# Kernel optimization log

Hardware: AMD Instinct MI355X
Metric: run time of the kernel (lower is better)

## Reference

```python
import jax, jax.numpy as jnp
import numpy as np

CLIP = 16          # relative_clip
REL = 2 * CLIP + 1 # relative_size = 33
NEG = 1e9


def setup_inputs() -> dict:
    key = jax.random.key(0)
    k1, k2, k3, k4, k5 = jax.random.split(key, 5)
    B, L, D = 8, 2048, 64
    return {
        "query": jax.random.normal(k1, (B, L, D), jnp.float32),
        "key": jax.random.normal(k2, (B, L, D), jnp.float32),
        "value": jax.random.normal(k3, (B, L, D), jnp.float32),
        "mask": jnp.ones((B, 1, L), jnp.float32),
        "key_relative": jax.random.normal(k4, (REL, D), jnp.float32),
        "value_relative": jax.random.normal(k5, (REL, D), jnp.float32),
    }


def reference(query, key, value, mask, key_relative, value_relative):
    B, Q, Dk = query.shape
    K = key.shape[1]
    scale = jnp.asarray(np.sqrt(Dk), query.dtype)

    # dot products [B,Q,K] (torch code does broadcast-mul+sum; matmul is same math)
    dot = jnp.einsum('bqd,bkd->bqk', query, key)

    # relative key bias: dot_relative [B,Q,REL], gathered by diag_id[q,k]
    dot_rel = jnp.einsum('bqd,td->bqt', query, key_relative)
    qi = jnp.arange(Q)[:, None]
    kj = jnp.arange(K)[None, :]
    diag_id = jnp.clip(qi - kj + CLIP, 0, 2 * CLIP)           # [Q,K]
    rel_bias = jnp.take_along_axis(
        dot_rel, jnp.broadcast_to(diag_id[None], (B, Q, K)), axis=2)
    dot = dot + rel_bias

    # only_attend_front: causal mask (strict upper triangle penalized)
    causal = jnp.triu(jnp.ones((K, K), dot.dtype), 1) * NEG   # [K,K]
    dot = dot - causal[None]

    # padding mask (broadcast)
    dot = dot - (1.0 - mask) * NEG

    logits = dot / scale
    probs = jax.nn.softmax(logits, axis=-1)
    # zero rows where every position is masked out
    n_masked = jnp.sum(dot <= -5e8, axis=-1, keepdims=True)
    probs = probs * (n_masked < K).astype(probs.dtype)
    # dropout with droprate=0.0 / eval mode -> identity

    res = jnp.einsum('bqk,bkd->bqd', probs, value)

    # relative value recombination: recover_id[q,r] = q + r - CLIP, OOB -> K (zero col)
    recover = jnp.arange(Q)[:, None] + jnp.arange(REL)[None, :] - CLIP  # [Q,REL]
    recover = jnp.where((recover < 0) | (recover >= K), K, recover)
    probs_pad = jnp.concatenate(
        [probs, jnp.zeros((B, Q, 1), probs.dtype)], axis=-1)           # [B,Q,K+1]
    rel_probs = jnp.take_along_axis(
        probs_pad, jnp.broadcast_to(recover[None], (B, Q, REL)), axis=2)
    res = res + jnp.einsum('bqr,rd->bqd', rel_probs, value_relative)
    return res
```

## Files before the change

### kernel.cpp

```cpp
#include <hip/hip_runtime.h>

typedef __attribute__((ext_vector_type(4))) float f32x4;
typedef __attribute__((ext_vector_type(8))) short s16x8;
typedef __attribute__((ext_vector_type(4))) short s16x4;

#define LSEQ 2048
#define NB   8
#define CH   8
#define UPB  80
#define NUNIT 640

#define QSCALE   0.180336880f
#define PENSCALE 1.8033688e8f

#define OFF_QB    0x000000u
#define OFF_KB    0x200000u
#define OFF_VTB   0x400000u
#define OFF_PEN   0x600000u
#define OFF_KREL  0x610000u
#define OFF_OPART 0x620000u
#define OFF_ML    0x1020000u

__device__ __forceinline__ unsigned short f2bf(float f) {
    union { float f; unsigned int u; } v; v.f = f;
    unsigned int u = v.u;
    return (unsigned short)((u + 0x7fffu + ((u >> 16) & 1u)) >> 16);
}

__device__ __forceinline__ float bf2f(unsigned short b) {
    union { unsigned int u; float f; } v; v.u = ((unsigned int)b) << 16;
    return v.f;
}

__global__ __launch_bounds__(256)
void convert_kernel(const float* __restrict__ Q, const float* __restrict__ K,
                    const float* __restrict__ V, const float* __restrict__ Msk,
                    const float* __restrict__ Krel, char* __restrict__ ws)
{
    const int tid = threadIdx.x;
    const int bid = blockIdx.x;
    unsigned short* Qb  = (unsigned short*)(ws + OFF_QB);
    unsigned short* Kb  = (unsigned short*)(ws + OFF_KB);
    unsigned short* VTb = (unsigned short*)(ws + OFF_VTB);
    float*          pen = (float*)(ws + OFF_PEN);
    unsigned short* Krb = (unsigned short*)(ws + OFF_KREL);

    if (bid < 1024) {
        int base = bid * 1024 + tid * 4;
        f32x4 q4 = *(const f32x4*)(Q + base);
        s16x4 o;
        o.x = (short)f2bf(q4.x * QSCALE); o.y = (short)f2bf(q4.y * QSCALE);
        o.z = (short)f2bf(q4.z * QSCALE); o.w = (short)f2bf(q4.w * QSCALE);
        *(s16x4*)(Qb + base) = o;
    } else if (bid < 2048) {
        int base = (bid - 1024) * 1024 + tid * 4;
        f32x4 k4 = *(const f32x4*)(K + base);
        s16x4 o;
        o.x = (short)f2bf(k4.x); o.y = (short)f2bf(k4.y);
        o.z = (short)f2bf(k4.z); o.w = (short)f2bf(k4.w);
        *(s16x4*)(Kb + base) = o;
    } else if (bid < 2304) {
        __shared__ unsigned short tileT[64][72];
        int tile = bid - 2048;
        int b = tile >> 5, k0 = (tile & 31) << 6;
        #pragma unroll
        for (int rep = 0; rep < 4; ++rep) {
            int idx = tid + rep * 256;
            int kr = idx >> 4, dc0 = (idx & 15) << 2;
            f32x4 v4 = *(const f32x4*)(V + (size_t)(b * 2048 + k0 + kr) * 64 + dc0);
            tileT[dc0 + 0][kr] = f2bf(v4.x);
            tileT[dc0 + 1][kr] = f2bf(v4.y);
            tileT[dc0 + 2][kr] = f2bf(v4.z);
            tileT[dc0 + 3][kr] = f2bf(v4.w);
        }
        __syncthreads();
        #pragma unroll
        for (int rep = 0; rep < 2; ++rep) {
            int idx = tid + rep * 256;
            int d = idx >> 3, ch = idx & 7;
            *(s16x8*)(VTb + (size_t)(b * 64 + d) * 2048 + k0 + ch * 8) =
                *(const s16x8*)&tileT[d][ch * 8];
        }
    } else if (bid < 2312) {
        int i0 = (bid - 2304) * 2048 + tid * 8;
        f32x4 m0 = *(const f32x4*)(Msk + i0);
        f32x4 m1 = *(const f32x4*)(Msk + i0 + 4);
        f32x4 p0 = (m0 - 1.0f) * PENSCALE;
        f32x4 p1 = (m1 - 1.0f) * PENSCALE;
        *(f32x4*)(pen + i0) = p0;
        *(f32x4*)(pen + i0 + 4) = p1;
    } else {
        for (int g = tid; g < 768; g += 256) {
            int e = g * 4, row = e >> 6, col = e & 63;
            s16x4 o;
            if (row < 33) {
                f32x4 v = *(const f32x4*)(Krel + row * 64 + col);
                o.x = (short)f2bf(v.x); o.y = (short)f2bf(v.y);
                o.z = (short)f2bf(v.z); o.w = (short)f2bf(v.w);
            } else {
                o.x = 0; o.y = 0; o.z = 0; o.w = 0;
            }
            *(s16x4*)(Krb + row * 64 + col) = o;
        }
    }
}

#define LDS_BUF0 0
#define LDS_BUF1 16640
#define LDS_P    33280
#define LDS_DREL 41472
#define LDS_VREL 46592
#define LDS_TOT  51488

#define SGB __builtin_amdgcn_sched_group_barrier
#define M_DSRD 0x100
#define M_MFMA 0x008

__device__ __forceinline__ void near_bias(f32x4& sv, const f32x4& pv, int cc,
                                          int k0, int g0, int q,
                                          const float* drel) {
#pragma unroll
    for (int r = 0; r < 4; ++r) {
        int kk = k0 + cc * 16 + 4 * g0 + r;
        int dlt = q - kk;
        int idx = dlt < 16 ? dlt : 16;
        idx = idx < 0 ? 0 : idx;
        float bb = drel[idx];
        float v = sv[r] + bb + pv[r];
        sv[r] = (dlt < 0) ? -1e30f : v;
    }
}

__global__ __launch_bounds__(256, 3)
void attn_main(const float* __restrict__ Vrel_g, float* __restrict__ Out,
               char* __restrict__ ws)
{
    __shared__ __align__(16) char lds[LDS_TOT];
    const int tid  = threadIdx.x;
    const int wv   = tid >> 6;
    const int lane = tid & 63;
    const int g0   = lane >> 4;
    const int qh   = lane & 15;

    int u = blockIdx.x;
    int b = u / UPB;
    int u2 = u - b * UPB;
    int t, chunk, nck;
    if (u2 < 8)       { t = u2;               chunk = 0;          nck = 1; }
    else if (u2 < 24) { t = 8  + (u2 - 8) / 2;  chunk = (u2 - 8) & 1;  nck = 2; }
    else if (u2 < 48) { t = 16 + (u2 - 24) / 3; chunk = (u2 - 24) % 3; nck = 3; }
    else              { t = 24 + (u2 - 48) / 4; chunk = (u2 - 48) & 3; nck = 4; }
    const int q0   = t << 6;
    const int q0w  = q0 + wv * 16;
    const int q    = q0w + qh;
    const int ck0  = chunk * CH;
    const int ckend = min(ck0 + CH, t + 1);
    const bool is_final = (nck == 1);

    const unsigned short* Qb  = (const unsigned short*)(ws + OFF_QB);
    const unsigned short* Kb  = (const unsigned short*)(ws + OFF_KB);
    const unsigned short* VTb = (const unsigned short*)(ws + OFF_VTB);
    const float*          pen = (const float*)(ws + OFF_PEN);
    const unsigned short* Krb = (const unsigned short*)(ws + OFF_KREL);

    const size_t qrow = (size_t)(b * 2048 + q) * 64;
    s16x8 qf0 = *(const s16x8*)(Qb + qrow + 0 * 32 + g0 * 8);
    s16x8 qf1 = *(const s16x8*)(Qb + qrow + 1 * 32 + g0 * 8);

    {
        s16x8 a10 = *(const s16x8*)(Krb + (16 + qh) * 64 + 0 * 32 + g0 * 8);
        s16x8 a11 = *(const s16x8*)(Krb + (16 + qh) * 64 + 1 * 32 + g0 * 8);
        s16x8 a20 = *(const s16x8*)(Krb + (32 + qh) * 64 + 0 * 32 + g0 * 8);
        s16x8 a21 = *(const s16x8*)(Krb + (32 + qh) * 64 + 1 * 32 + g0 * 8);
        f32x4 z = {0.f, 0.f, 0.f, 0.f};
        f32x4 d1 = __builtin_amdgcn_mfma_f32_16x16x32_bf16(a10, qf0, z, 0, 0, 0);
        d1 = __builtin_amdgcn_mfma_f32_16x16x32_bf16(a11, qf1, d1, 0, 0, 0);
        f32x4 d2 = __builtin_amdgcn_mfma_f32_16x16x32_bf16(a20, qf0, z, 0, 0, 0);
        d2 = __builtin_amdgcn_mfma_f32_16x16x32_bf16(a21, qf1, d2, 0, 0, 0);
        float* drel = (float*)(lds + LDS_DREL) + wv * 320 + qh * 20;
        drel[4 * g0 + 0] = d1.x; drel[4 * g0 + 1] = d1.y;
        drel[4 * g0 + 2] = d1.z; drel[4 * g0 + 3] = d1.w;
        if (g0 == 0) drel[16] = d2.x;
    }
    asm volatile("" ::: "memory");
    const float* drelT = (const float*)(lds + LDS_DREL) + wv * 320 + qh * 20;
    float bias32 = drelT[16];

    {
        float* vr = (float*)(lds + LDS_VREL);
        for (int i = tid; i < 17 * 16; i += 256) {
            int row = i >> 4, c4 = (i & 15) << 2;
            *(f32x4*)(vr + row * 72 + c4) = *(const f32x4*)(Vrel_g + row * 64 + c4);
        }
    }

    f32x4 o0 = {0,0,0,0}, o1 = {0,0,0,0}, o2 = {0,0,0,0}, o3 = {0,0,0,0};
    float mprev = -1e30f, lsum = 0.f;

    char* PL  = lds + LDS_P + wv * 2048;
    const int swzq = (qh & 7) << 4;
    const float* vrel = (const float*)(lds + LDS_VREL);

    const int idx0 = tid,        idx1 = tid + 256;
    const int row0 = idx0 >> 3,  cb0 = (idx0 & 7) << 4;
    const int row1 = idx1 >> 3,  cb1 = (idx1 & 7) << 4;
    const int sw0 = cb0 ^ ((row0 & 7) << 4);
    const int sw1 = cb1 ^ ((row1 & 7) << 4);
    const char* ksrc0 = (const char*)(Kb  + (size_t)(b * 2048 + row0) * 64) + cb0;
    const char* ksrc1 = (const char*)(Kb  + (size_t)(b * 2048 + row1) * 64) + cb1;
    const char* vsrc0 = (const char*)(VTb + (size_t)(b * 64 + row0) * 2048) + cb0;
    const char* vsrc1 = (const char*)(VTb + (size_t)(b * 64 + row1) * 2048) + cb1;
    const float* psrc = pen + b * 2048 + (tid << 2);

    s16x8 rk0, rk1, rv0, rv1;
    f32x4 rpen;
#define LOADREGS(KT)                                                          \
    do {                                                                      \
        rk0 = *(const s16x8*)(ksrc0 + (size_t)(KT) * 8192);                   \
        rk1 = *(const s16x8*)(ksrc1 + (size_t)(KT) * 8192);                   \
        rv0 = *(const s16x8*)(vsrc0 + (size_t)(KT) * 128);                    \
        rv1 = *(const s16x8*)(vsrc1 + (size_t)(KT) * 128);                    \
        if (tid < 16) rpen = *(const f32x4*)(psrc + ((KT) << 6));             \
    } while (0)
#define STOREREGS(BASE)                                                       \
    do {                                                                      \
        *(s16x8*)((BASE) + row0 * 128 + sw0) = rk0;                           \
        *(s16x8*)((BASE) + row1 * 128 + sw1) = rk1;                           \
        *(s16x8*)((BASE) + 8192 + row0 * 128 + sw0) = rv0;                    \
        *(s16x8*)((BASE) + 8192 + row1 * 128 + sw1) = rv1;                    \
        if (tid < 16) *(f32x4*)((BASE) + 16384 + (tid << 4)) = rpen;          \
    } while (0)

    LOADREGS(ck0);
    STOREREGS(lds + LDS_BUF0);

    const int nkt = ckend - ck0;
    for (int it = 0; it < nkt; ++it) {
        const int kt = ck0 + it;
        const int k0 = kt << 6;
        const int cur = it & 1;
        const bool havenext = (it + 1 < nkt);
        if (havenext) LOADREGS(kt + 1);
        __syncthreads();

        char* KsL = lds + (cur ? LDS_BUF1 : LDS_BUF0);
        char* VtL = KsL + 8192;
        const float* pf = (const float*)(KsL + 16384);

        if (k0 <= q0w + 15) {
            const int b0 = (16 * g0) ^ swzq;
            const int b1 = (64 + 16 * g0) ^ swzq;
            f32x4 s0, s1, s2, s3;
            {
                f32x4 z = {0,0,0,0};
                s16x8 a0 = *(const s16x8*)(KsL + (0  + qh) * 128 + b0);
                s16x8 a1 = *(const s16x8*)(KsL + (0  + qh) * 128 + b1);
                s16x8 a2 = *(const s16x8*)(KsL + (16 + qh) * 128 + b0);
                s16x8 a3 = *(const s16x8*)(KsL + (16 + qh) * 128 + b1);
                s0 = __builtin_amdgcn_mfma_f32_16x16x32_bf16(a0, qf0, z, 0, 0, 0);
                s0 = __builtin_amdgcn_mfma_f32_16x16x32_bf16(a1, qf1, s0, 0, 0, 0);
                a0 = *(const s16x8*)(KsL + (32 + qh) * 128 + b0);
                a1 = *(const s16x8*)(KsL + (32 + qh) * 128 + b1);
                s1 = __builtin_amdgcn_mfma_f32_16x16x32_bf16(a2, qf0, z, 0, 0, 0);
                s1 = __builtin_amdgcn_mfma_f32_16x16x32_bf16(a3, qf1, s1, 0, 0, 0);
                a2 = *(const s16x8*)(KsL + (48 + qh) * 128 + b0);
                a3 = *(const s16x8*)(KsL + (48 + qh) * 128 + b1);
                s2 = __builtin_amdgcn_mfma_f32_16x16x32_bf16(a0, qf0, z, 0, 0, 0);
                s2 = __builtin_amdgcn_mfma_f32_16x16x32_bf16(a1, qf1, s2, 0, 0, 0);
                s3 = __builtin_amdgcn_mfma_f32_16x16x32_bf16(a2, qf0, z, 0, 0, 0);
                s3 = __builtin_amdgcn_mfma_f32_16x16x32_bf16(a3, qf1, s3, 0, 0, 0);
                SGB(M_DSRD, 4, 0); SGB(M_MFMA, 2, 0);
                SGB(M_DSRD, 2, 0); SGB(M_MFMA, 2, 0);
                SGB(M_DSRD, 2, 0); SGB(M_MFMA, 2, 0);
                SGB(M_MFMA, 2, 0);
            }
            f32x4 pn0 = *(const f32x4*)(pf + 4 * g0);
            f32x4 pn1 = *(const f32x4*)(pf + 16 + 4 * g0);
            f32x4 pn2 = *(const f32x4*)(pf + 32 + 4 * g0);
            f32x4 pn3 = *(const f32x4*)(pf + 48 + 4 * g0);
            const bool near = (k0 + 79 >= q0w);
            if (!near) {
                s0 += pn0 + bias32; s1 += pn1 + bias32;
                s2 += pn2 + bias32; s3 += pn3 + bias32;
            } else {
                near_bias(s0, pn0, 0, k0, g0, q, drelT);
                near_bias(s1, pn1, 1, k0, g0, q, drelT);
                near_bias(s2, pn2, 2, k0, g0, q, drelT);
                near_bias(s3, pn3, 3, k0, g0, q, drelT);
            }
            float mt = fmaxf(fmaxf(fmaxf(s0.x, s0.y), fmaxf(s0.z, s0.w)),
                      fmaxf(fmaxf(fmaxf(s1.x, s1.y), fmaxf(s1.z, s1.w)),
                      fmaxf(fmaxf(fmaxf(s2.x, s2.y), fmaxf(s2.z, s2.w)),
                            fmaxf(fmaxf(s3.x, s3.y), fmaxf(s3.z, s3.w)))));
            mt = fmaxf(mt, __shfl_xor(mt, 16));
            mt = fmaxf(mt, __shfl_xor(mt, 32));
            float mnew = fmaxf(mprev, mt);
            float fsc = __builtin_amdgcn_exp2f(mprev - mnew);
            s0.x = __builtin_amdgcn_exp2f(s0.x - mnew); s0.y = __builtin_amdgcn_exp2f(s0.y - mnew);
            s0.z = __builtin_amdgcn_exp2f(s0.z - mnew); s0.w = __builtin_amdgcn_exp2f(s0.w - mnew);
            s1.x = __builtin_amdgcn_exp2f(s1.x - mnew); s1.y = __builtin_amdgcn_exp2f(s1.y - mnew);
            s1.z = __builtin_amdgcn_exp2f(s1.z - mnew); s1.w = __builtin_amdgcn_exp2f(s1.w - mnew);
            s2.x = __builtin_amdgcn_exp2f(s2.x - mnew); s2.y = __builtin_amdgcn_exp2f(s2.y - mnew);
            s2.z = __builtin_amdgcn_exp2f(s2.z - mnew); s2.w = __builtin_amdgcn_exp2f(s2.w - mnew);
            s3.x = __builtin_amdgcn_exp2f(s3.x - mnew); s3.y = __builtin_amdgcn_exp2f(s3.y - mnew);
            s3.z = __builtin_amdgcn_exp2f(s3.z - mnew); s3.w = __builtin_amdgcn_exp2f(s3.w - mnew);
            float rs = (s0.x + s0.y + s0.z + s0.w) + (s1.x + s1.y + s1.z + s1.w)
                     + (s2.x + s2.y + s2.z + s2.w) + (s3.x + s3.y + s3.z + s3.w);
            rs += __shfl_xor(rs, 16);
            rs += __shfl_xor(rs, 32);
            lsum = lsum * fsc + rs;
            mprev = mnew;
            o0 *= fsc; o1 *= fsc; o2 *= fsc; o3 *= fsc;

            {
                s16x4 pk;
                pk.x = (short)f2bf(s0.x); pk.y = (short)f2bf(s0.y);
                pk.z = (short)f2bf(s0.z); pk.w = (short)f2bf(s0.w);
                *(s16x4*)(PL + qh * 128 + ((0  + 8 * g0) ^ swzq)) = pk;
                pk.x = (short)f2bf(s1.x); pk.y = (short)f2bf(s1.y);
                pk.z = (short)f2bf(s1.z); pk.w = (short)f2bf(s1.w);
                *(s16x4*)(PL + qh * 128 + ((32 + 8 * g0) ^ swzq)) = pk;
                pk.x = (short)f2bf(s2.x); pk.y = (short)f2bf(s2.y);
                pk.z = (short)f2bf(s2.z); pk.w = (short)f2bf(s2.w);
                *(s16x4*)(PL + qh * 128 + ((64 + 8 * g0) ^ swzq)) = pk;
                pk.x = (short)f2bf(s3.x); pk.y = (short)f2bf(s3.y);
                pk.z = (short)f2bf(s3.z); pk.w = (short)f2bf(s3.w);
                *(s16x4*)(PL + qh * 128 + ((96 + 8 * g0) ^ swzq)) = pk;
            }
            asm volatile("" ::: "memory");
            {
                s16x8 bP0 = *(const s16x8*)(PL + qh * 128 + b0);
                s16x8 bP1 = *(const s16x8*)(PL + qh * 128 + b1);
                s16x8 v0 = *(const s16x8*)(VtL + (0  + qh) * 128 + b0);
                s16x8 v1 = *(const s16x8*)(VtL + (0  + qh) * 128 + b1);
                s16x8 v2 = *(const s16x8*)(VtL + (16 + qh) * 128 + b0);
                s16x8 v3 = *(const s16x8*)(VtL + (16 + qh) * 128 + b1);
                o0 = __builtin_amdgcn_mfma_f32_16x16x32_bf16(v0, bP0, o0, 0, 0, 0);
                o0 = __builtin_amdgcn_mfma_f32_16x16x32_bf16(v1, bP1, o0, 0, 0, 0);
                v0 = *(const s16x8*)(VtL + (32 + qh) * 128 + b0);
                v1 = *(const s16x8*)(VtL + (32 + qh) * 128 + b1);
                o1 = __builtin_amdgcn_mfma_f32_16x16x32_bf16(v2, bP0, o1, 0, 0, 0);
                o1 = __builtin_amdgcn_mfma_f32_16x16x32_bf16(v3, bP1, o1, 0, 0, 0);
                v2 = *(const s16x8*)(VtL + (48 + qh) * 128 + b0);
                v3 = *(const s16x8*)(VtL + (48 + qh) * 128 + b1);
                o2 = __builtin_amdgcn_mfma_f32_16x16x32_bf16(v0, bP0, o2, 0, 0, 0);
                o2 = __builtin_amdgcn_mfma_f32_16x16x32_bf16(v1, bP1, o2, 0, 0, 0);
                o3 = __builtin_amdgcn_mfma_f32_16x16x32_bf16(v2, bP0, o3, 0, 0, 0);
                o3 = __builtin_amdgcn_mfma_f32_16x16x32_bf16(v3, bP1, o3, 0, 0, 0);
                SGB(M_DSRD, 6, 1); SGB(M_MFMA, 2, 1);
                SGB(M_DSRD, 2, 1); SGB(M_MFMA, 2, 1);
                SGB(M_DSRD, 2, 1); SGB(M_MFMA, 2, 1);
                SGB(M_MFMA, 2, 1);
            }
            if (near) {
                const int kql = q - k0;
                #pragma unroll
                for (int dlt = 0; dlt <= 16; ++dlt) {
                    int kkl = kql - dlt;
                    if (kkl >= 0 && kkl < 64) {
                        float p = bf2f(*(const unsigned short*)
                                       (PL + qh * 128 + ((2 * kkl) ^ swzq)));
                        const float* vrow = vrel + (16 - dlt) * 72 + 4 * g0;
                        o0 += p * *(const f32x4*)(vrow + 0);
                        o1 += p * *(const f32x4*)(vrow + 16);
                        o2 += p * *(const f32x4*)(vrow + 32);
                        o3 += p * *(const f32x4*)(vrow + 48);
                    }
                }
            }
        }

        if (havenext) {
            STOREREGS(lds + ((cur ^ 1) ? LDS_BUF1 : LDS_BUF0));
        }
    }

    if (is_final) {
        float inv = 1.f / lsum;
        float* op = Out + (size_t)(b * 2048 + q) * 64 + 4 * g0;
        *(f32x4*)(op + 0)  = o0 * inv;
        *(f32x4*)(op + 16) = o1 * inv;
        *(f32x4*)(op + 32) = o2 * inv;
        *(f32x4*)(op + 48) = o3 * inv;
    } else {
        float* op = (float*)(ws + OFF_OPART) + (size_t)u * 4096 + (wv * 16 + qh) * 64 + 4 * g0;
        *(f32x4*)(op + 0)  = o0;
        *(f32x4*)(op + 16) = o1;
        *(f32x4*)(op + 32) = o2;
        *(f32x4*)(op + 48) = o3;
        if (g0 == 0) {
            float* ml = (float*)(ws + OFF_ML) + (size_t)u * 128 + (wv * 16 + qh) * 2;
            ml[0] = mprev; ml[1] = lsum;
        }
    }
}

__global__ __launch_bounds__(256)
void combine_kernel(float* __restrict__ Out, const char* __restrict__ ws)
{
    int bid = blockIdx.x;
    int b = bid / 24;
    int t = 8 + bid % 24;
    int nck = t / 8 + 1;
    int S;
    if (t < 16)      S = 8 + 2 * (t - 8);
    else if (t < 24) S = 24 + 3 * (t - 16);
    else             S = 48 + 4 * (t - 24);
    int ubase = b * UPB + S;
    int tid = threadIdx.x;
    int qloc = tid >> 2;
    int d0 = (tid & 3) << 4;
    const float* mlb = (const float*)(ws + OFF_ML);
    const float* opb = (const float*)(ws + OFF_OPART);

    float m[4], l[4];
    float M = -1e30f;
    #pragma unroll
    for (int i = 0; i < 4; ++i) {
        if (i < nck) {
            const float* ml = mlb + (size_t)(ubase + i) * 128 + qloc * 2;
            m[i] = ml[0]; l[i] = ml[1];
            M = fmaxf(M, m[i]);
        }
    }
    float L = 0.f;
    float coef[4];
    #pragma unroll
    for (int i = 0; i < 4; ++i) {
        if (i < nck) { coef[i] = __builtin_amdgcn_exp2f(m[i] - M); L += l[i] * coef[i]; }
    }
    f32x4 a0 = {0,0,0,0}, a1 = {0,0,0,0}, a2 = {0,0,0,0}, a3 = {0,0,0,0};
    #pragma unroll
    for (int i = 0; i < 4; ++i) {
        if (i < nck) {
            const float* op = opb + (size_t)(ubase + i) * 4096 + qloc * 64 + d0;
            a0 += coef[i] * *(const f32x4*)(op + 0);
            a1 += coef[i] * *(const f32x4*)(op + 4);
            a2 += coef[i] * *(const f32x4*)(op + 8);
            a3 += coef[i] * *(const f32x4*)(op + 12);
        }
    }
    float inv = 1.f / L;
    float* oo = Out + (size_t)(b * 2048 + t * 64 + qloc) * 64 + d0;
    *(f32x4*)(oo + 0)  = a0 * inv;
    *(f32x4*)(oo + 4)  = a1 * inv;
    *(f32x4*)(oo + 8)  = a2 * inv;
    *(f32x4*)(oo + 12) = a3 * inv;
}

extern "C" void kernel_launch(void* const* d_in, const int* in_sizes, int n_in,
                              void* d_out, int out_size, void* d_ws, size_t ws_size,
                              hipStream_t stream) {
    (void)in_sizes; (void)n_in; (void)out_size; (void)ws_size;
    const float* Q    = (const float*)d_in[0];
    const float* K    = (const float*)d_in[1];
    const float* V    = (const float*)d_in[2];
    const float* Msk  = (const float*)d_in[3];
    const float* Krel = (const float*)d_in[4];
    const float* Vrel = (const float*)d_in[5];
    float* Out = (float*)d_out;
    char* ws = (char*)d_ws;

    convert_kernel<<<2313, 256, 0, stream>>>(Q, K, V, Msk, Krel, ws);
    attn_main<<<NUNIT, 256, 0, stream>>>(Vrel, Out, ws);
    attn_main<<<NUNIT, 256, 0, stream>>>(Vrel, Out, ws);
    combine_kernel<<<192, 256, 0, stream>>>(Out, ws);
}
```

Baseline: 126.8 us.

## Load K/V fragments directly from global, drop LDS staging and duplicate launch

Result: slower. 132.1 us (+4.2%).

```diff
diff --git a/kernel.cpp b/kernel.cpp
--- a/kernel.cpp
+++ b/kernel.cpp
@@ -3,6 +3,7 @@
 typedef __attribute__((ext_vector_type(4))) float f32x4;
 typedef __attribute__((ext_vector_type(8))) short s16x8;
 typedef __attribute__((ext_vector_type(4))) short s16x4;
+typedef __attribute__((ext_vector_type(2))) unsigned int u32x2;
 
 #define LSEQ 2048
 #define NB   8
@@ -30,6 +31,12 @@
 __device__ __forceinline__ float bf2f(unsigned short b) {
     union { unsigned int u; float f; } v; v.u = ((unsigned int)b) << 16;
     return v.f;
+}
+
+__device__ __forceinline__ unsigned int cvtpk(float lo, float hi) {
+    unsigned int r;
+    asm("v_cvt_pk_bf16_f32 %0, %1, %2" : "=v"(r) : "v"(lo), "v"(hi));
+    return r;
 }
 
 __global__ __launch_bounds__(256)
@@ -105,16 +112,10 @@
     }
 }
 
-#define LDS_BUF0 0
-#define LDS_BUF1 16640
-#define LDS_P    33280
-#define LDS_DREL 41472
-#define LDS_VREL 46592
-#define LDS_TOT  51488
-
-#define SGB __builtin_amdgcn_sched_group_barrier
-#define M_DSRD 0x100
-#define M_MFMA 0x008
+#define LDS_P    0
+#define LDS_DREL 8192
+#define LDS_VREL 13312
+#define LDS_TOT  18208
 
 __device__ __forceinline__ void near_bias(f32x4& sv, const f32x4& pv, int cc,
                                           int k0, int g0, int q,
@@ -131,7 +132,7 @@
     }
 }
 
-__global__ __launch_bounds__(256, 3)
+__global__ __launch_bounds__(256, 4)
 void attn_main(const float* __restrict__ Vrel_g, float* __restrict__ Out,
                char* __restrict__ ws)
 {
@@ -142,7 +143,7 @@
     const int g0   = lane >> 4;
     const int qh   = lane & 15;
 
-    int u = blockIdx.x;
+    int u = (blockIdx.x & 7) * UPB + (blockIdx.x >> 3);
     int b = u / UPB;
     int u2 = u - b * UPB;
     int t, chunk, nck;
@@ -193,6 +194,7 @@
             *(f32x4*)(vr + row * 72 + c4) = *(const f32x4*)(Vrel_g + row * 64 + c4);
         }
     }
+    __syncthreads();
 
     f32x4 o0 = {0,0,0,0}, o1 = {0,0,0,0}, o2 = {0,0,0,0}, o3 = {0,0,0,0};
     float mprev = -1e30f, lsum = 0.f;
@@ -201,177 +203,124 @@
     const int swzq = (qh & 7) << 4;
     const float* vrel = (const float*)(lds + LDS_VREL);
 
-    const int idx0 = tid,        idx1 = tid + 256;
-    const int row0 = idx0 >> 3,  cb0 = (idx0 & 7) << 4;
-    const int row1 = idx1 >> 3,  cb1 = (idx1 & 7) << 4;
-    const int sw0 = cb0 ^ ((row0 & 7) << 4);
-    const int sw1 = cb1 ^ ((row1 & 7) << 4);
-    const char* ksrc0 = (const char*)(Kb  + (size_t)(b * 2048 + row0) * 64) + cb0;
-    const char* ksrc1 = (const char*)(Kb  + (size_t)(b * 2048 + row1) * 64) + cb1;
-    const char* vsrc0 = (const char*)(VTb + (size_t)(b * 64 + row0) * 2048) + cb0;
-    const char* vsrc1 = (const char*)(VTb + (size_t)(b * 64 + row1) * 2048) + cb1;
-    const float* psrc = pen + b * 2048 + (tid << 2);
-
-    s16x8 rk0, rk1, rv0, rv1;
-    f32x4 rpen;
-#define LOADREGS(KT)                                                          \
-    do {                                                                      \
-        rk0 = *(const s16x8*)(ksrc0 + (size_t)(KT) * 8192);                   \
-        rk1 = *(const s16x8*)(ksrc1 + (size_t)(KT) * 8192);                   \
-        rv0 = *(const s16x8*)(vsrc0 + (size_t)(KT) * 128);                    \
-        rv1 = *(const s16x8*)(vsrc1 + (size_t)(KT) * 128);                    \
-        if (tid < 16) rpen = *(const f32x4*)(psrc + ((KT) << 6));             \
-    } while (0)
-#define STOREREGS(BASE)                                                       \
-    do {                                                                      \
-        *(s16x8*)((BASE) + row0 * 128 + sw0) = rk0;                           \
-        *(s16x8*)((BASE) + row1 * 128 + sw1) = rk1;                           \
-        *(s16x8*)((BASE) + 8192 + row0 * 128 + sw0) = rv0;                    \
-        *(s16x8*)((BASE) + 8192 + row1 * 128 + sw1) = rv1;                    \
-        if (tid < 16) *(f32x4*)((BASE) + 16384 + (tid << 4)) = rpen;          \
-    } while (0)
-
-    LOADREGS(ck0);
-    STOREREGS(lds + LDS_BUF0);
-
-    const int nkt = ckend - ck0;
-    for (int it = 0; it < nkt; ++it) {
-        const int kt = ck0 + it;
+    const unsigned short* kfb = Kb  + (size_t)(b * 2048 + qh) * 64 + g0 * 8;
+    const unsigned short* vfb = VTb + (size_t)(b * 64 + qh) * 2048 + g0 * 8;
+
+    for (int kt = ck0; kt < ckend; ++kt) {
         const int k0 = kt << 6;
-        const int cur = it & 1;
-        const bool havenext = (it + 1 < nkt);
-        if (havenext) LOADREGS(kt + 1);
-        __syncthreads();
-
-        char* KsL = lds + (cur ? LDS_BUF1 : LDS_BUF0);
-        char* VtL = KsL + 8192;
-        const float* pf = (const float*)(KsL + 16384);
-
-        if (k0 <= q0w + 15) {
+        if (k0 > q0w + 15) continue;
+
+        const unsigned short* kf = kfb + (size_t)k0 * 64;
+        f32x4 s0, s1, s2, s3;
+        {
+            f32x4 z = {0,0,0,0};
+            s16x8 a0 = *(const s16x8*)(kf + 0 * 1024 + 0);
+            s16x8 a1 = *(const s16x8*)(kf + 0 * 1024 + 32);
+            s16x8 a2 = *(const s16x8*)(kf + 1 * 1024 + 0);
+            s16x8 a3 = *(const s16x8*)(kf + 1 * 1024 + 32);
+            s0 = __builtin_amdgcn_mfma_f32_16x16x32_bf16(a0, qf0, z, 0, 0, 0);
+            s0 = __builtin_amdgcn_mfma_f32_16x16x32_bf16(a1, qf1, s0, 0, 0, 0);
+            a0 = *(const s16x8*)(kf + 2 * 1024 + 0);
+            a1 = *(const s16x8*)(kf + 2 * 1024 + 32);
+            s1 = __builtin_amdgcn_mfma_f32_16x16x32_bf16(a2, qf0, z, 0, 0, 0);
+            s1 = __builtin_amdgcn_mfma_f32_16x16x32_bf16(a3, qf1, s1, 0, 0, 0);
+            a2 = *(const s16x8*)(kf + 3 * 1024 + 0);
+            a3 = *(const s16x8*)(kf + 3 * 1024 + 32);
+            s2 = __builtin_amdgcn_mfma_f32_16x16x32_bf16(a0, qf0, z, 0, 0, 0);
+            s2 = __builtin_amdgcn_mfma_f32_16x16x32_bf16(a1, qf1, s2, 0, 0, 0);
+            s3 = __builtin_amdgcn_mfma_f32_16x16x32_bf16(a2, qf0, z, 0, 0, 0);
+            s3 = __builtin_amdgcn_mfma_f32_16x16x32_bf16(a3, qf1, s3, 0, 0, 0);
+        }
+        const float* penb = pen + b * 2048 + k0 + 4 * g0;
+        f32x4 pn0 = *(const f32x4*)(penb + 0);
+        f32x4 pn1 = *(const f32x4*)(penb + 16);
+        f32x4 pn2 = *(const f32x4*)(penb + 32);
+        f32x4 pn3 = *(const f32x4*)(penb + 48);
+        const bool near = (k0 + 79 >= q0w);
+        if (!near) {
+            s0 += pn0 + bias32; s1 += pn1 + bias32;
+            s2 += pn2 + bias32; s3 += pn3 + bias32;
+        } else {
+            near_bias(s0, pn0, 0, k0, g0, q, drelT);
+            near_bias(s1, pn1, 1, k0, g0, q, drelT);
+            near_bias(s2, pn2, 2, k0, g0, q, drelT);
+            near_bias(s3, pn3, 3, k0, g0, q, drelT);
+        }
+        float mt = fmaxf(fmaxf(fmaxf(s0.x, s0.y), fmaxf(s0.z, s0.w)),
+                  fmaxf(fmaxf(fmaxf(s1.x, s1.y), fmaxf(s1.z, s1.w)),
+                  fmaxf(fmaxf(fmaxf(s2.x, s2.y), fmaxf(s2.z, s2.w)),
+                        fmaxf(fmaxf(s3.x, s3.y), fmaxf(s3.z, s3.w)))));
+        mt = fmaxf(mt, __shfl_xor(mt, 16));
+        mt = fmaxf(mt, __shfl_xor(mt, 32));
+        float mnew = fmaxf(mprev, mt);
+        float fsc = __builtin_amdgcn_exp2f(mprev - mnew);
+        s0.x = __builtin_amdgcn_exp2f(s0.x - mnew); s0.y = __builtin_amdgcn_exp2f(s0.y - mnew);
+        s0.z = __builtin_amdgcn_exp2f(s0.z - mnew); s0.w = __builtin_amdgcn_exp2f(s0.w - mnew);
+        s1.x = __builtin_amdgcn_exp2f(s1.x - mnew); s1.y = __builtin_amdgcn_exp2f(s1.y - mnew);
+        s1.z = __builtin_amdgcn_exp2f(s1.z - mnew); s1.w = __builtin_amdgcn_exp2f(s1.w - mnew);
+        s2.x = __builtin_amdgcn_exp2f(s2.x - mnew); s2.y = __builtin_amdgcn_exp2f(s2.y - mnew);
+        s2.z = __builtin_amdgcn_exp2f(s2.z - mnew); s2.w = __builtin_amdgcn_exp2f(s2.w - mnew);
+        s3.x = __builtin_amdgcn_exp2f(s3.x - mnew); s3.y = __builtin_amdgcn_exp2f(s3.y - mnew);
+        s3.z = __builtin_amdgcn_exp2f(s3.z - mnew); s3.w = __builtin_amdgcn_exp2f(s3.w - mnew);
+        float rs = (s0.x + s0.y + s0.z + s0.w) + (s1.x + s1.y + s1.z + s1.w)
+                 + (s2.x + s2.y + s2.z + s2.w) + (s3.x + s3.y + s3.z + s3.w);
+        rs += __shfl_xor(rs, 16);
+        rs += __shfl_xor(rs, 32);
+        lsum = lsum * fsc + rs;
+        mprev = mnew;
+        o0 *= fsc; o1 *= fsc; o2 *= fsc; o3 *= fsc;
+
+        {
+            u32x2 pk;
+            pk.x = cvtpk(s0.x, s0.y); pk.y = cvtpk(s0.z, s0.w);
+            *(u32x2*)(PL + qh * 128 + ((0  + 8 * g0) ^ swzq)) = pk;
+            pk.x = cvtpk(s1.x, s1.y); pk.y = cvtpk(s1.z, s1.w);
+            *(u32x2*)(PL + qh * 128 + ((32 + 8 * g0) ^ swzq)) = pk;
+            pk.x = cvtpk(s2.x, s2.y); pk.y = cvtpk(s2.z, s2.w);
+            *(u32x2*)(PL + qh * 128 + ((64 + 8 * g0) ^ swzq)) = pk;
+            pk.x = cvtpk(s3.x, s3.y); pk.y = cvtpk(s3.z, s3.w);
+            *(u32x2*)(PL + qh * 128 + ((96 + 8 * g0) ^ swzq)) = pk;
+        }
+        asm volatile("" ::: "memory");
+        {
             const int b0 = (16 * g0) ^ swzq;
             const int b1 = (64 + 16 * g0) ^ swzq;
-            f32x4 s0, s1, s2, s3;
-            {
-                f32x4 z = {0,0,0,0};
-                s16x8 a0 = *(const s16x8*)(KsL + (0  + qh) * 128 + b0);
-                s16x8 a1 = *(const s16x8*)(KsL + (0  + qh) * 128 + b1);
-                s16x8 a2 = *(const s16x8*)(KsL + (16 + qh) * 128 + b0);
-                s16x8 a3 = *(const s16x8*)(KsL + (16 + qh) * 128 + b1);
-                s0 = __builtin_amdgcn_mfma_f32_16x16x32_bf16(a0, qf0, z, 0, 0, 0);
-                s0 = __builtin_amdgcn_mfma_f32_16x16x32_bf16(a1, qf1, s0, 0, 0, 0);
-                a0 = *(const s16x8*)(KsL + (32 + qh) * 128 + b0);
-                a1 = *(const s16x8*)(KsL + (32 + qh) * 128 + b1);
-                s1 = __builtin_amdgcn_mfma_f32_16x16x32_bf16(a2, qf0, z, 0, 0, 0);
-                s1 = __builtin_amdgcn_mfma_f32_16x16x32_bf16(a3, qf1, s1, 0, 0, 0);
-                a2 = *(const s16x8*)(KsL + (48 + qh) * 128 + b0);
-                a3 = *(const s16x8*)(KsL + (48 + qh) * 128 + b1);
-                s2 = __builtin_amdgcn_mfma_f32_16x16x32_bf16(a0, qf0, z, 0, 0, 0);
-                s2 = __builtin_amdgcn_mfma_f32_16x16x32_bf16(a1, qf1, s2, 0, 0, 0);
-                s3 = __builtin_amdgcn_mfma_f32_16x16x32_bf16(a2, qf0, z, 0, 0, 0);
-                s3 = __builtin_amdgcn_mfma_f32_16x16x32_bf16(a3, qf1, s3, 0, 0, 0);
-                SGB(M_DSRD, 4, 0); SGB(M_MFMA, 2, 0);
-                SGB(M_DSRD, 2, 0); SGB(M_MFMA, 2, 0);
-                SGB(M_DSRD, 2, 0); SGB(M_MFMA, 2, 0);
-                SGB(M_MFMA, 2, 0);
-            }
-            f32x4 pn0 = *(const f32x4*)(pf + 4 * g0);
-            f32x4 pn1 = *(const f32x4*)(pf + 16 + 4 * g0);
-            f32x4 pn2 = *(const f32x4*)(pf + 32 + 4 * g0);
-            f32x4 pn3 = *(const f32x4*)(pf + 48 + 4 * g0);
-            const bool near = (k0 + 79 >= q0w);
-            if (!near) {
-                s0 += pn0 + bias32; s1 += pn1 + bias32;
-                s2 += pn2 + bias32; s3 += pn3 + bias32;
-            } else {
-                near_bias(s0, pn0, 0, k0, g0, q, drelT);
-                near_bias(s1, pn1, 1, k0, g0, q, drelT);
-                near_bias(s2, pn2, 2, k0, g0, q, drelT);
-                near_bias(s3, pn3, 3, k0, g0, q, drelT);
-            }
-            float mt = fmaxf(fmaxf(fmaxf(s0.x, s0.y), fmaxf(s0.z, s0.w)),
-                      fmaxf(fmaxf(fmaxf(s1.x, s1.y), fmaxf(s1.z, s1.w)),
-                      fmaxf(fmaxf(fmaxf(s2.x, s2.y), fmaxf(s2.z, s2.w)),
-                            fmaxf(fmaxf(s3.x, s3.y), fmaxf(s3.z, s3.w)))));
-            mt = fmaxf(mt, __shfl_xor(mt, 16));
-            mt = fmaxf(mt, __shfl_xor(mt, 32));
-            float mnew = fmaxf(mprev, mt);
-            float fsc = __builtin_amdgcn_exp2f(mprev - mnew);
-            s0.x = __builtin_amdgcn_exp2f(s0.x - mnew); s0.y = __builtin_amdgcn_exp2f(s0.y - mnew);
-            s0.z = __builtin_amdgcn_exp2f(s0.z - mnew); s0.w = __builtin_amdgcn_exp2f(s0.w - mnew);
-            s1.x = __builtin_amdgcn_exp2f(s1.x - mnew); s1.y = __builtin_amdgcn_exp2f(s1.y - mnew);
-            s1.z = __builtin_amdgcn_exp2f(s1.z - mnew); s1.w = __builtin_amdgcn_exp2f(s1.w - mnew);
-            s2.x = __builtin_amdgcn_exp2f(s2.x - mnew); s2.y = __builtin_amdgcn_exp2f(s2.y - mnew);
-            s2.z = __builtin_amdgcn_exp2f(s2.z - mnew); s2.w = __builtin_amdgcn_exp2f(s2.w - mnew);
-            s3.x = __builtin_amdgcn_exp2f(s3.x - mnew); s3.y = __builtin_amdgcn_exp2f(s3.y - mnew);
-            s3.z = __builtin_amdgcn_exp2f(s3.z - mnew); s3.w = __builtin_amdgcn_exp2f(s3.w - mnew);
-            float rs = (s0.x + s0.y + s0.z + s0.w) + (s1.x + s1.y + s1.z + s1.w)
-                     + (s2.x + s2.y + s2.z + s2.w) + (s3.x + s3.y + s3.z + s3.w);
-            rs += __shfl_xor(rs, 16);
-            rs += __shfl_xor(rs, 32);
-            lsum = lsum * fsc + rs;
-            mprev = mnew;
-            o0 *= fsc; o1 *= fsc; o2 *= fsc; o3 *= fsc;
-
-            {
-                s16x4 pk;
-                pk.x = (short)f2bf(s0.x); pk.y = (short)f2bf(s0.y);
-                pk.z = (short)f2bf(s0.z); pk.w = (short)f2bf(s0.w);
-                *(s16x4*)(PL + qh * 128 + ((0  + 8 * g0) ^ swzq)) = pk;
-                pk.x = (short)f2bf(s1.x); pk.y = (short)f2bf(s1.y);
-                pk.z = (short)f2bf(s1.z); pk.w = (short)f2bf(s1.w);
-                *(s16x4*)(PL + qh * 128 + ((32 + 8 * g0) ^ swzq)) = pk;
-                pk.x = (short)f2bf(s2.x); pk.y = (short)f2bf(s2.y);
-                pk.z = (short)f2bf(s2.z); pk.w = (short)f2bf(s2.w);
-                *(s16x4*)(PL + qh * 128 + ((64 + 8 * g0) ^ swzq)) = pk;
-                pk.x = (short)f2bf(s3.x); pk.y = (short)f2bf(s3.y);
-                pk.z = (short)f2bf(s3.z); pk.w = (short)f2bf(s3.w);
-                *(s16x4*)(PL + qh * 128 + ((96 + 8 * g0) ^ swzq)) = pk;
-            }
+            s16x8 bP0 = *(const s16x8*)(PL + qh * 128 + b0);
+            s16x8 bP1 = *(const s16x8*)(PL + qh * 128 + b1);
             asm volatile("" ::: "memory");
-            {
-                s16x8 bP0 = *(const s16x8*)(PL + qh * 128 + b0);
-                s16x8 bP1 = *(const s16x8*)(PL + qh * 128 + b1);
-                s16x8 v0 = *(const s16x8*)(VtL + (0  + qh) * 128 + b0);
-                s16x8 v1 = *(const s16x8*)(VtL + (0  + qh) * 128 + b1);
-                s16x8 v2 = *(const s16x8*)(VtL + (16 + qh) * 128 + b0);
-                s16x8 v3 = *(const s16x8*)(VtL + (16 + qh) * 128 + b1);
-                o0 = __builtin_amdgcn_mfma_f32_16x16x32_bf16(v0, bP0, o0, 0, 0, 0);
-                o0 = __builtin_amdgcn_mfma_f32_16x16x32_bf16(v1, bP1, o0, 0, 0, 0);
-                v0 = *(const s16x8*)(VtL + (32 + qh) * 128 + b0);
-                v1 = *(const s16x8*)(VtL + (32 + qh) * 128 + b1);
-                o1 = __builtin_amdgcn_mfma_f32_16x16x32_bf16(v2, bP0, o1, 0, 0, 0);
-                o1 = __builtin_amdgcn_mfma_f32_16x16x32_bf16(v3, bP1, o1, 0, 0, 0);
-                v2 = *(const s16x8*)(VtL + (48 + qh) * 128 + b0);
-                v3 = *(const s16x8*)(VtL + (48 + qh) * 128 + b1);
-                o2 = __builtin_amdgcn_mfma_f32_16x16x32_bf16(v0, bP0, o2, 0, 0, 0);
-                o2 = __builtin_amdgcn_mfma_f32_16x16x32_bf16(v1, bP1, o2, 0, 0, 0);
-                o3 = __builtin_amdgcn_mfma_f32_16x16x32_bf16(v2, bP0, o3, 0, 0, 0);
-                o3 = __builtin_amdgcn_mfma_f32_16x16x32_bf16(v3, bP1, o3, 0, 0, 0);
-                SGB(M_DSRD, 6, 1); SGB(M_MFMA, 2, 1);
-                SGB(M_DSRD, 2, 1); SGB(M_MFMA, 2, 1);
-                SGB(M_DSRD, 2, 1); SGB(M_MFMA, 2, 1);
-                SGB(M_MFMA, 2, 1);
-            }
-            if (near) {
-                const int kql = q - k0;
-                #pragma unroll
-                for (int dlt = 0; dlt <= 16; ++dlt) {
-                    int kkl = kql - dlt;
-                    if (kkl >= 0 && kkl < 64) {
-                        float p = bf2f(*(const unsigned short*)
-                                       (PL + qh * 128 + ((2 * kkl) ^ swzq)));
-                        const float* vrow = vrel + (16 - dlt) * 72 + 4 * g0;
-                        o0 += p * *(const f32x4*)(vrow + 0);
-                        o1 += p * *(const f32x4*)(vrow + 16);
-                        o2 += p * *(const f32x4*)(vrow + 32);
-                        o3 += p * *(const f32x4*)(vrow + 48);
-                    }
+            const unsigned short* vf = vfb + k0;
+            s16x8 v0 = *(const s16x8*)(vf + 0 * 32768 + 0);
+            s16x8 v1 = *(const s16x8*)(vf + 0 * 32768 + 32);
+            s16x8 v2 = *(const s16x8*)(vf + 1 * 32768 + 0);
+            s16x8 v3 = *(const s16x8*)(vf + 1 * 32768 + 32);
+            o0 = __builtin_amdgcn_mfma_f32_16x16x32_bf16(v0, bP0, o0, 0, 0, 0);
+            o0 = __builtin_amdgcn_mfma_f32_16x16x32_bf16(v1, bP1, o0, 0, 0, 0);
+            v0 = *(const s16x8*)(vf + 2 * 32768 + 0);
+            v1 = *(const s16x8*)(vf + 2 * 32768 + 32);
+            o1 = __builtin_amdgcn_mfma_f32_16x16x32_bf16(v2, bP0, o1, 0, 0, 0);
+            o1 = __builtin_amdgcn_mfma_f32_16x16x32_bf16(v3, bP1, o1, 0, 0, 0);
+            v2 = *(const s16x8*)(vf + 3 * 32768 + 0);
+            v3 = *(const s16x8*)(vf + 3 * 32768 + 32);
+            o2 = __builtin_amdgcn_mfma_f32_16x16x32_bf16(v0, bP0, o2, 0, 0, 0);
+            o2 = __builtin_amdgcn_mfma_f32_16x16x32_bf16(v1, bP1, o2, 0, 0, 0);
+            o3 = __builtin_amdgcn_mfma_f32_16x16x32_bf16(v2, bP0, o3, 0, 0, 0);
+            o3 = __builtin_amdgcn_mfma_f32_16x16x32_bf16(v3, bP1, o3, 0, 0, 0);
+        }
+        if (near) {
+            const int kql = q - k0;
+            #pragma unroll
+            for (int dlt = 0; dlt <= 16; ++dlt) {
+                int kkl = kql - dlt;
+                if (kkl >= 0 && kkl < 64) {
+                    float p = bf2f(*(const unsigned short*)
+                                   (PL + qh * 128 + ((2 * kkl) ^ swzq)));
+                    const float* vrow = vrel + (16 - dlt) * 72 + 4 * g0;
+                    o0 += p * *(const f32x4*)(vrow + 0);
+                    o1 += p * *(const f32x4*)(vrow + 16);
+                    o2 += p * *(const f32x4*)(vrow + 32);
+                    o3 += p * *(const f32x4*)(vrow + 48);
                 }
             }
-        }
-
-        if (havenext) {
-            STOREREGS(lds + ((cur ^ 1) ? LDS_BUF1 : LDS_BUF0));
         }
     }
 
@@ -463,6 +412,5 @@
 
     convert_kernel<<<2313, 256, 0, stream>>>(Q, K, V, Msk, Krel, ws);
     attn_main<<<NUNIT, 256, 0, stream>>>(Vrel, Out, ws);
-    attn_main<<<NUNIT, 256, 0, stream>>>(Vrel, Out, ws);
     combine_kernel<<<192, 256, 0, stream>>>(Out, ws);
 }
```
